# Performance work log

Hardware: AMD Instinct MI355X
Metric: run time of the kernel (lower is better)

## Reference

```python
import math
import jax, jax.numpy as jnp
import numpy as np

N_HEADS = 8
N_POINTS = 4


def bilinear_sample(img, gx, gy):
    """torch F.grid_sample(bilinear, align_corners=True, padding='zeros').
    img: [N,C,H,W]; gx,gy: [N,P] normalized coords (gx -> width axis, gy -> height axis).
    Returns [N,C,P]."""
    N, C, H, W = img.shape
    ix = (gx + 1.0) * 0.5 * (W - 1)
    iy = (gy + 1.0) * 0.5 * (H - 1)
    x0 = jnp.floor(ix); y0 = jnp.floor(iy)
    x1 = x0 + 1.0;      y1 = y0 + 1.0

    def corner(yc, xc, w):
        m = (xc >= 0) & (xc <= W - 1) & (yc >= 0) & (yc <= H - 1)
        xi = jnp.clip(xc, 0, W - 1).astype(jnp.int32)
        yi = jnp.clip(yc, 0, H - 1).astype(jnp.int32)
        v = jax.vmap(lambda im, y, x: im[:, y, x])(img, yi, xi)  # [N,C,P]
        return v * (w * m)[:, None, :]

    return (corner(y0, x0, (x1 - ix) * (y1 - iy))
            + corner(y0, x1, (ix - x0) * (y1 - iy))
            + corner(y1, x0, (x1 - ix) * (iy - y0))
            + corner(y1, x1, (ix - x0) * (iy - y0)))


def forward(query, points, features, cam_M, cam_b, W_off, b_off,
            W_q, b_q, W_k, b_k, W_v, b_v, W_o, b_o):
    B, K, C = query.shape
    ncam = features.shape[0]
    H, W = features.shape[-2:]
    nh, npnt = N_HEADS, N_POINTS
    hd = C // nh
    HW = jnp.asarray([H, W], dtype=query.dtype)

    # camera model: pixel = sigmoid(points @ M^T + b) * [H, W]   -> [ncam,B,K,2]
    px = jax.nn.sigmoid(jnp.einsum('bkj,cij->cbki', points, cam_M)
                        + cam_b[:, None, None, :]) * HW

    # ---- step 1: sample raw features at projected points (per camera) ----
    # original normalizes coord0 by H and coord1 by W (coord0 is grid_sample's x/width axis)
    gx1 = 2.0 * px[..., 0] / H - 1.0          # [ncam,B,K]
    gy1 = 2.0 * px[..., 1] / W - 1.0
    camf = jax.vmap(bilinear_sample)(features, gx1, gy1)   # [ncam,B,C,K]
    camf = jnp.transpose(camf, (1, 3, 0, 2))               # [B,K,ncam,C]

    query_ = query[:, :, None, :] + camf                   # [B,K,ncam,C]
    offsets = (query_ @ W_off.T + b_off).reshape(B, K, ncam, nh, npnt, 2)

    # ---- 1x1 conv key/value projections ----
    kf = (jnp.einsum('cbdhw,ed->cbehw', features, W_k)
          + b_k[None, None, :, None, None]).reshape(ncam, B * nh, hd, H, W)
    vf = (jnp.einsum('cbdhw,ed->cbehw', features, W_v)
          + b_v[None, None, :, None, None]).reshape(ncam, B * nh, hd, H, W)

    # ---- sampling locations with offsets ----
    off = jnp.moveaxis(offsets, 2, 0) / HW                 # [ncam,B,K,nh,np,2]
    pc = px[:, :, :, None, None, :] + off                  # [ncam,B,K,nh,np,2]
    gx = 2.0 * (pc[..., 0] / H) - 1.0
    gy = 2.0 * (pc[..., 1] / W) - 1.0
    # [ncam,B,K,nh,np] -> [ncam, B*nh, K*np]
    gx = jnp.transpose(gx, (0, 1, 3, 2, 4)).reshape(ncam, B * nh, K * npnt)
    gy = jnp.transpose(gy, (0, 1, 3, 2, 4)).reshape(ncam, B * nh, K * npnt)

    keys = jax.vmap(bilinear_sample)(kf, gx, gy)           # [ncam,B*nh,hd,K*np]
    vals = jax.vmap(bilinear_sample)(vf, gx, gy)

    def rearr(t):  # -> [B, nh, K, ncam*np, hd]
        t = t.reshape(ncam, B, nh, hd, K, npnt)
        return jnp.transpose(t, (1, 2, 4, 0, 5, 3)).reshape(B, nh, K, ncam * npnt, hd)

    keys, vals = rearr(keys), rearr(vals)

    q = (query @ W_q.T + b_q).reshape(B, K, nh, hd).transpose(0, 2, 1, 3)  # [B,nh,K,hd]
    logits = jnp.einsum('bhkd,bhkld->bhkl', q, keys) / math.sqrt(hd)
    attn = jax.nn.softmax(logits, axis=-1)
    weighted = jnp.einsum('bhkl,bhkld->bhkd', attn, vals)  # [B,nh,K,hd]
    # faithful to original torch `.view(B, K, embed_dim)` on a [B,nh,K,hd] tensor
    weighted = weighted.reshape(B, K, C)
    return weighted @ W_o.T + b_o


def setup_inputs() -> dict:
    key = jax.random.key(0)
    ks = jax.random.split(key, 16)
    B, K, C = 8, 900, 256
    ncam, H, W = 6, 32, 88
    f = lambda i, shape, s=1.0: jax.random.normal(ks[i], shape, dtype=jnp.float32) * s
    return {
        'query': f(0, (B, K, C)),
        'points': f(1, (B, K, 3)),
        'features': f(2, (ncam, B, C, H, W)),
        'cam_M': f(3, (ncam, 2, 3), 0.5),
        'cam_b': f(4, (ncam, 2), 0.5),
        'W_off': f(5, (2 * N_HEADS * N_POINTS, C), 0.02),
        'b_off': f(6, (2 * N_HEADS * N_POINTS,), 1.0),
        'W_q': f(7, (C, C), 0.02), 'b_q': f(8, (C,), 0.02),
        'W_k': f(9, (C, C), 0.02), 'b_k': f(10, (C,), 0.02),
        'W_v': f(11, (C, C), 0.02), 'b_v': f(12, (C,), 0.02),
        'W_o': f(13, (C, C), 0.02), 'b_o': f(14, (C,), 0.02),
    }


def reference(query, points, features, cam_M, cam_b, W_off, b_off,
              W_q, b_q, W_k, b_k, W_v, b_v, W_o, b_o):
    return forward(query, points, features, cam_M, cam_b, W_off, b_off,
                   W_q, b_q, W_k, b_k, W_v, b_v, W_o, b_o)
```

## Files before the change

### kernel.cpp

```cpp
#include <hip/hip_runtime.h>

typedef __attribute__((ext_vector_type(4))) float f32x4;
typedef __attribute__((ext_vector_type(8))) short bf16x8;
typedef __attribute__((ext_vector_type(4))) unsigned int u32x4;

__device__ __forceinline__ unsigned short f2bf(float f) {
    union { float f; unsigned int u; } x; x.f = f;
    unsigned int u = x.u;
    return (unsigned short)((u + 0x7FFFu + ((u >> 16) & 1u)) >> 16);
}
__device__ __forceinline__ float bf2f(unsigned short b) {
    union { unsigned int u; float f; } x; x.u = ((unsigned int)b) << 16;
    return x.f;
}
__device__ __forceinline__ float u2f(unsigned int u) {
    union { unsigned int u; float f; } x; x.u = u; return x.f;
}


__global__ void prep_all(const float* __restrict__ Wk, const float* __restrict__ bk,
                         const float* __restrict__ Wv, const float* __restrict__ bv,
                         const float* __restrict__ Wq, const float* __restrict__ bq,
                         const float* __restrict__ Woff, const float* __restrict__ boff,
                         unsigned short* __restrict__ Wkv, float* __restrict__ bkv,
                         unsigned short* __restrict__ Woffp,
                         float* __restrict__ Wcat, float* __restrict__ bcat) {
    int i = blockIdx.x * 256 + threadIdx.x;
    if (i < 512 * 256) {
        int n = i >> 8, k = i & 255;
        float v = (n < 256) ? Wk[i] : Wv[i - 65536];
        Wkv[((size_t)(n >> 7) * 8 + (k >> 5)) * 4096 + (n & 127) * 32 + (k & 31)] = f2bf(v);
    }
    if (i < 512) bkv[i] = (i < 256) ? bk[i] : bv[i - 256];
    if (i < 64 * 256) {
        int n = i >> 8, k = i & 255;
        Woffp[(size_t)(k >> 5) * 4096 + n * 32 + (k & 31)] = f2bf(Woff[i]);
    }
    if (i < 320 * 256) Wcat[i] = (i < 65536) ? Wq[i] : Woff[i - 65536];
    if (i < 320) bcat[i] = (i < 256) ? bq[i] : boff[i - 256];
}

__global__ __launch_bounds__(256) void transpose_feat(const float* __restrict__ src,
                                                      unsigned short* __restrict__ dst) {
    __shared__ float tile[32][33];
    int img = blockIdx.z;
    int p0 = blockIdx.x * 32;
    int d0 = blockIdx.y * 32;
    int tx = threadIdx.x & 31, ty = threadIdx.x >> 5;
    const float* s = src + (size_t)img * 256 * 2816;
#pragma unroll
    for (int i = 0; i < 4; i++) tile[ty + 8 * i][tx] = s[(size_t)(d0 + ty + 8 * i) * 2816 + p0 + tx];
    __syncthreads();
    int m = img * 2816 + p0;
    unsigned short* o = dst + ((size_t)(m >> 7) * 8 + (d0 >> 5)) * 4096 + (m & 127) * 32;
#pragma unroll
    for (int i = 0; i < 4; i++) o[(ty + 8 * i) * 32 + tx] = f2bf(tile[tx][ty + 8 * i]);
}

__global__ __launch_bounds__(256) void gemm_kv2(
    const unsigned short* __restrict__ A,
    const unsigned short* __restrict__ Wkv,
    const unsigned short* __restrict__ Woffp,
    const float* __restrict__ bias,
    unsigned short* __restrict__ C,
    float* __restrict__ Foff) {
    __shared__ __align__(16) unsigned short Bl[8192];
    __shared__ __align__(16) unsigned short Ar[3][4096];

    const int tid = threadIdx.x, lane = tid & 63, w = tid >> 6;
    const int lrow = lane & 15, lk = lane >> 4;
    const int lsw = (lane >> 2) * 32 + (((lane & 3) ^ ((lane >> 3) & 3)) * 8);
    const int ckx = ((lrow >> 1) & 3);
    const int bid = blockIdx.x;
    const int wgid = (bid & 7) * 1188 + (bid >> 3);
    const int chunk = wgid / 9, bn = wgid % 9;

    const unsigned short* A0 = A + (size_t)chunk * 32768;
    const unsigned short* Bb = (bn < 8)
        ? Wkv + (size_t)(bn >> 1) * 32768 + (bn & 1) * 2048
        : Woffp;
    const int wof = w * 1024;

#define STAGE_B(HALF)                                                                        \
    {                                                                                        \
        _Pragma("unroll")                                                                    \
        for (int i = 0; i < 4; ++i) {                                                        \
            __builtin_amdgcn_global_load_lds(                                                \
                (const __attribute__((address_space(1))) unsigned int*)(Bb + ((HALF) * 4 + w) * 4096 + i * 512 + lsw), \
                (__attribute__((address_space(3))) unsigned int*)&Bl[w * 2048 + i * 512], 16, 0, 0);                   \
        }                                                                                    \
    }

#define STAGE_STEP(S)                                                                        \
    {                                                                                        \
        __builtin_amdgcn_global_load_lds(                                                    \
            (const __attribute__((address_space(1))) unsigned int*)(A0 + (S) * 4096 + wof + lsw),        \
            (__attribute__((address_space(3))) unsigned int*)&Ar[(S) % 3][wof], 16, 0, 0);   \
        __builtin_amdgcn_global_load_lds(                                                    \
            (const __attribute__((address_space(1))) unsigned int*)(A0 + (S) * 4096 + wof + 512 + lsw),  \
            (__attribute__((address_space(3))) unsigned int*)&Ar[(S) % 3][wof + 512], 16, 0, 0);         \
    }

    STAGE_B(0)
    STAGE_STEP(0) STAGE_STEP(1)
    __syncthreads();

    f32x4 acc[2][4] = {};

#define COMP_STEP(S, NW)                                                                     \
    {                                                                                        \
        asm volatile("s_waitcnt vmcnt(%0)" :: "i"(NW) : "memory");                           \
        bf16x8 bfr[4], af[2];                                                                \
        _Pragma("unroll") for (int j = 0; j < 4; ++j)                                        \
            bfr[j] = *(const bf16x8*)&Bl[((S) & 3) * 2048 + (j * 16 + lrow) * 32 + (lk ^ ckx) * 8]; \
        _Pragma("unroll") for (int i = 0; i < 2; ++i)                                        \
            af[i] = *(const bf16x8*)&Ar[(S) % 3][wof + i * 512 + lrow * 32 + (lk ^ ckx) * 8];\
        if ((S) + 2 < 8) {                                                                   \
            asm volatile("s_waitcnt lgkmcnt(0)" ::: "memory");                               \
            STAGE_STEP((S) + 2)                                                              \
        }                                                                                    \
        _Pragma("unroll") for (int i = 0; i < 2; ++i)                                        \
            _Pragma("unroll") for (int j = 0; j < 4; ++j)                                    \
                acc[i][j] = __builtin_amdgcn_mfma_f32_16x16x32_bf16(af[i], bfr[j], acc[i][j], 0, 0, 0); \
    }

    COMP_STEP(0, 4) COMP_STEP(1, 2) COMP_STEP(2, 2) COMP_STEP(3, 2)
    __syncthreads();
    STAGE_B(1)
    __syncthreads();
    COMP_STEP(4, 4) COMP_STEP(5, 2) COMP_STEP(6, 2) COMP_STEP(7, 0)
#undef COMP_STEP
#undef STAGE_STEP
#undef STAGE_B

    if (bn < 8) {
        unsigned short* Cl = &Ar[0][0];
        __syncthreads();
#pragma unroll
        for (int j = 0; j < 4; ++j) {
            float bs = bias[bn * 64 + j * 16 + lrow];
#pragma unroll
            for (int i = 0; i < 2; ++i)
#pragma unroll
                for (int jj = 0; jj < 4; ++jj)
                    Cl[(w * 32 + i * 16 + lk * 4 + jj) * 64 + j * 16 + lrow] =
                        f2bf(acc[i][j][jj] + bs);
        }
        __syncthreads();
#pragma unroll
        for (int it = 0; it < 4; ++it) {
            int idx = it * 256 + tid;
            int row = idx >> 3, col8 = idx & 7;
            int dstcol = (bn < 4)
                ? (bn * 2 + (col8 >> 2)) * 64 + (col8 & 3) * 8
                : ((bn - 4) * 2 + (col8 >> 2)) * 64 + 32 + (col8 & 3) * 8;
            *(f32x4*)(C + (size_t)(chunk * 128 + row) * 512 + dstcol) =
                *(const f32x4*)&Cl[row * 64 + col8 * 8];
        }
    } else {
#pragma unroll
        for (int i = 0; i < 2; ++i)
#pragma unroll
            for (int j = 0; j < 4; ++j)
#pragma unroll
                for (int jj = 0; jj < 4; ++jj) {
                    int m = chunk * 128 + w * 32 + i * 16 + lk * 4 + jj;
                    Foff[(size_t)m * 64 + j * 16 + lrow] = acc[i][j][jj];
                }
    }
}

template <bool SPLIT, bool C_BF16>
__global__ __launch_bounds__(256) void gemm_bf16(
    const float* __restrict__ A, long long aBatch,
    const float* __restrict__ B, const float* __restrict__ bias,
    void* __restrict__ Cv, long long cBatch,
    int M, int N, int K, int lda) {
    __shared__ __align__(16) unsigned short Ah[64][40];
    __shared__ __align__(16) unsigned short Bh[64][40];
    __shared__ __align__(16) unsigned short Al[(SPLIT ? 64 : 1)][40];
    __shared__ __align__(16) unsigned short Bl[(SPLIT ? 64 : 1)][40];

    const int tid = threadIdx.x;
    const int m0 = blockIdx.x * 64, n0 = blockIdx.y * 64;
    const int batch = blockIdx.z;
    const float* Ab = A + (size_t)batch * aBatch;
    const int lane = tid & 63, wave = tid >> 6;
    const int wr = wave & 1, wc = wave >> 1;
    const int lrow = lane & 15, lk = lane >> 4;

    f32x4 acc[2][2] = {};

    for (int kt = 0; kt < K; kt += 32) {
        if (kt) __syncthreads();
        {
            int c4 = (tid & 7) * 4;
#pragma unroll
            for (int rep = 0; rep < 2; rep++) {
                int r = (tid >> 3) + rep * 32;
                int m = m0 + r; if (m >= M) m = M - 1;
                f32x4 v = *(const f32x4*)(Ab + (size_t)m * lda + kt + c4);
#pragma unroll
                for (int q = 0; q < 4; q++) {
                    unsigned short h = f2bf(v[q]);
                    Ah[r][c4 + q] = h;
                    if (SPLIT) Al[r][c4 + q] = f2bf(v[q] - bf2f(h));
                }
            }
        }
        {
            int c4 = (tid & 7) * 4;
#pragma unroll
            for (int rep = 0; rep < 2; rep++) {
                int r = (tid >> 3) + rep * 32;
                f32x4 v = *(const f32x4*)(B + (size_t)(n0 + r) * K + kt + c4);
#pragma unroll
                for (int q = 0; q < 4; q++) {
                    unsigned short h = f2bf(v[q]);
                    Bh[r][c4 + q] = h;
                    if (SPLIT) Bl[r][c4 + q] = f2bf(v[q] - bf2f(h));
                }
            }
        }
        __syncthreads();

        bf16x8 a_h[2], b_h[2], a_l[2], b_l[2];
#pragma unroll
        for (int i = 0; i < 2; i++) {
            a_h[i] = *(const bf16x8*)&Ah[wr * 32 + i * 16 + lrow][lk * 8];
            b_h[i] = *(const bf16x8*)&Bh[wc * 32 + i * 16 + lrow][lk * 8];
            if (SPLIT) {
                a_l[i] = *(const bf16x8*)&Al[wr * 32 + i * 16 + lrow][lk * 8];
                b_l[i] = *(const bf16x8*)&Bl[wc * 32 + i * 16 + lrow][lk * 8];
            }
        }
#pragma unroll
        for (int i = 0; i < 2; i++)
#pragma unroll
            for (int j = 0; j < 2; j++) {
                acc[i][j] = __builtin_amdgcn_mfma_f32_16x16x32_bf16(a_h[i], b_h[j], acc[i][j], 0, 0, 0);
                if (SPLIT) {
                    acc[i][j] = __builtin_amdgcn_mfma_f32_16x16x32_bf16(a_h[i], b_l[j], acc[i][j], 0, 0, 0);
                    acc[i][j] = __builtin_amdgcn_mfma_f32_16x16x32_bf16(a_l[i], b_h[j], acc[i][j], 0, 0, 0);
                }
            }
    }

#pragma unroll
    for (int i = 0; i < 2; i++)
#pragma unroll
        for (int j = 0; j < 2; j++) {
            int n = n0 + wc * 32 + j * 16 + lrow;
            float bs = bias[n];
#pragma unroll
            for (int jj = 0; jj < 4; jj++) {
                int m = m0 + wr * 32 + i * 16 + lk * 4 + jj;
                if (m < M) {
                    float val = acc[i][j][jj] + bs;
                    if (C_BF16)
                        ((unsigned short*)Cv)[(size_t)batch * cBatch + (size_t)m * N + n] = f2bf(val);
                    else
                        ((float*)Cv)[(size_t)batch * cBatch + (size_t)m * N + n] = val;
                }
            }
        }
}

__global__ __launch_bounds__(512) void attn_kernel(
    const float* __restrict__ qcat, const float* __restrict__ points,
    const float* __restrict__ camM, const float* __restrict__ camb,
    const float* __restrict__ Foff, const unsigned short* __restrict__ kv_t,
    float* __restrict__ S) {
    int bk = blockIdx.x;
    int b = bk / 900, k = bk % 900;
    int h = threadIdx.x >> 6;
    int lane = threadIdx.x & 63;

    __shared__ __align__(16) float        ldsW[8][24][4];
    __shared__ __align__(16) unsigned int ldsI[8][24][4];
    __shared__ float ldsL[8][24];

    if (lane < 24) {
        int cam = lane >> 2, p = lane & 3;
        float pt0 = points[(size_t)bk * 3 + 0];
        float pt1 = points[(size_t)bk * 3 + 1];
        float pt2 = points[(size_t)bk * 3 + 2];
        const float* M = camM + cam * 6;
        float s0 = M[0] * pt0 + M[1] * pt1 + M[2] * pt2 + camb[cam * 2 + 0];
        float s1 = M[3] * pt0 + M[4] * pt1 + M[5] * pt2 + camb[cam * 2 + 1];
        float px0 = (1.f / (1.f + expf(-s0))) * 32.f;
        float px1 = (1.f / (1.f + expf(-s1))) * 88.f;
        {
            float gxb = 2.f * px0 / 32.f - 1.f, gyb = 2.f * px1 / 88.f - 1.f;
            float ixb = (gxb + 1.f) * 0.5f * 87.f;
            float iyb = (gyb + 1.f) * 0.5f * 31.f;
            float xb0 = floorf(ixb), yb0 = floorf(iyb), xb1 = xb0 + 1.f, yb1 = yb0 + 1.f;
            float wxb1 = ixb - xb0, wxb0 = xb1 - ixb, wyb1 = iyb - yb0, wyb0 = yb1 - iyb;
            float mb00 = (xb0 >= 0.f && xb0 <= 87.f && yb0 >= 0.f && yb0 <= 31.f) ? 1.f : 0.f;
            float mb01 = (xb1 >= 0.f && xb1 <= 87.f && yb0 >= 0.f && yb0 <= 31.f) ? 1.f : 0.f;
            float mb10 = (xb0 >= 0.f && xb0 <= 87.f && yb1 >= 0.f && yb1 <= 31.f) ? 1.f : 0.f;
            float mb11 = (xb1 >= 0.f && xb1 <= 87.f && yb1 >= 0.f && yb1 <= 31.f) ? 1.f : 0.f;
            float wb00 = wxb0 * wyb0 * mb00, wb01 = wxb1 * wyb0 * mb01;
            float wb10 = wxb0 * wyb1 * mb10, wb11 = wxb1 * wyb1 * mb11;
            int xib0 = (int)fminf(fmaxf(xb0, 0.f), 87.f);
            int xib1 = (int)fminf(fmaxf(xb1, 0.f), 87.f);
            int yib0 = (int)fminf(fmaxf(yb0, 0.f), 31.f);
            int yib1 = (int)fminf(fmaxf(yb1, 0.f), 31.f);
            size_t base = (size_t)(cam * 8 + b) * 2816;
            const float* f00 = Foff + (base + yib0 * 88 + xib0) * 64;
            const float* f01 = Foff + (base + yib0 * 88 + xib1) * 64;
            const float* f10 = Foff + (base + yib1 * 88 + xib0) * 64;
            const float* f11 = Foff + (base + yib1 * 88 + xib1) * 64;
            int j0 = (h * 4 + p) * 2;
            float o0 = qcat[(size_t)bk * 320 + 256 + j0]
                     + wb00 * f00[j0] + wb01 * f01[j0] + wb10 * f10[j0] + wb11 * f11[j0];
            float o1 = qcat[(size_t)bk * 320 + 256 + j0 + 1]
                     + wb00 * f00[j0 + 1] + wb01 * f01[j0 + 1] + wb10 * f10[j0 + 1] + wb11 * f11[j0 + 1];
            float pc0 = px0 + o0 * (1.f / 32.f);
            float pc1 = px1 + o1 * (1.f / 88.f);
            float gx = 2.f * (pc0 * (1.f / 32.f)) - 1.f;
            float gy = 2.f * (pc1 * (1.f / 88.f)) - 1.f;
            float ix = (gx + 1.f) * 0.5f * 87.f;
            float iy = (gy + 1.f) * 0.5f * 31.f;
            float x0 = floorf(ix), y0 = floorf(iy), x1 = x0 + 1.f, y1 = y0 + 1.f;
            float wx1 = ix - x0, wx0 = x1 - ix, wy1 = iy - y0, wy0 = y1 - iy;
            float m00 = (x0 >= 0.f && x0 <= 87.f && y0 >= 0.f && y0 <= 31.f) ? 1.f : 0.f;
            float m01 = (x1 >= 0.f && x1 <= 87.f && y0 >= 0.f && y0 <= 31.f) ? 1.f : 0.f;
            float m10 = (x0 >= 0.f && x0 <= 87.f && y1 >= 0.f && y1 <= 31.f) ? 1.f : 0.f;
            float m11 = (x1 >= 0.f && x1 <= 87.f && y1 >= 0.f && y1 <= 31.f) ? 1.f : 0.f;
            int xi0 = (int)fminf(fmaxf(x0, 0.f), 87.f);
            int xi1 = (int)fminf(fmaxf(x1, 0.f), 87.f);
            int yi0 = (int)fminf(fmaxf(y0, 0.f), 31.f);
            int yi1 = (int)fminf(fmaxf(y1, 0.f), 31.f);
            unsigned int img = (unsigned int)(cam * 8 + b) * 2816u;
            ldsW[h][lane][0] = wx0 * wy0 * m00;
            ldsW[h][lane][1] = wx1 * wy0 * m01;
            ldsW[h][lane][2] = wx0 * wy1 * m10;
            ldsW[h][lane][3] = wx1 * wy1 * m11;
            ldsI[h][lane][0] = (img + yi0 * 88 + xi0) * 1024u;
            ldsI[h][lane][1] = (img + yi0 * 88 + xi1) * 1024u;
            ldsI[h][lane][2] = (img + yi1 * 88 + xi0) * 1024u;
            ldsI[h][lane][3] = (img + yi1 * 88 + xi1) * 1024u;
        }
    }
    __syncthreads();

    const int p8 = lane >> 3, dlane = lane & 7;
    const int chB = h * 128 + dlane * 16;
    const char* kvb = (const char*)kv_t;

    f32x4 qa = *(const f32x4*)(qcat + (size_t)bk * 320 + h * 32 + (dlane & 3) * 8);
    f32x4 qb = *(const f32x4*)(qcat + (size_t)bk * 320 + h * 32 + (dlane & 3) * 8 + 4);

    float vr[3][8];
    const float inv_sqrt = 0.17677669529663687f;
#pragma unroll
    for (int it = 0; it < 3; ++it) {
        int l = it * 8 + p8;
        f32x4 w = *(const f32x4*)ldsW[h][l];
        unsigned int i0 = ldsI[h][l][0], i1 = ldsI[h][l][1];
        unsigned int i2 = ldsI[h][l][2], i3 = ldsI[h][l][3];
        u32x4 u0 = *(const u32x4*)(kvb + i0 + chB);
        u32x4 u1 = *(const u32x4*)(kvb + i1 + chB);
        u32x4 u2 = *(const u32x4*)(kvb + i2 + chB);
        u32x4 u3 = *(const u32x4*)(kvb + i3 + chB);
#pragma unroll
        for (int q = 0; q < 4; ++q) {
            vr[it][2 * q] = w[0] * u2f(u0[q] << 16) + w[1] * u2f(u1[q] << 16)
                          + w[2] * u2f(u2[q] << 16) + w[3] * u2f(u3[q] << 16);
            vr[it][2 * q + 1] = w[0] * u2f(u0[q] & 0xFFFF0000u) + w[1] * u2f(u1[q] & 0xFFFF0000u)
                              + w[2] * u2f(u2[q] & 0xFFFF0000u) + w[3] * u2f(u3[q] & 0xFFFF0000u);
        }
        float t = qa[0] * vr[it][0] + qa[1] * vr[it][1] + qa[2] * vr[it][2] + qa[3] * vr[it][3]
                + qb[0] * vr[it][4] + qb[1] * vr[it][5] + qb[2] * vr[it][6] + qb[3] * vr[it][7];
        t += __shfl_xor(t, 1);
        t += __shfl_xor(t, 2);
        if (dlane == 0) ldsL[h][l] = t * inv_sqrt;
    }
    __syncthreads();

    float mx = -1e30f;
#pragma unroll
    for (int l = 0; l < 24; l++) mx = fmaxf(mx, ldsL[h][l]);
    float ssum = 0.f;
    float at3[3];
#pragma unroll
    for (int l = 0; l < 24; l++) {
        float e = __expf(ldsL[h][l] - mx);
        ssum += e;
        if ((l & 7) == p8) at3[l >> 3] = e;
    }
    float inv = 1.f / ssum;

    float o[8];
#pragma unroll
    for (int j = 0; j < 8; ++j)
        o[j] = at3[0] * vr[0][j] + at3[1] * vr[1][j] + at3[2] * vr[2][j];
#pragma unroll
    for (int j = 0; j < 8; ++j) {
        o[j] += __shfl_xor(o[j], 8);
        o[j] += __shfl_xor(o[j], 16);
        o[j] += __shfl_xor(o[j], 32);
    }
    if (p8 == 0 && dlane >= 4) {
        int d0 = (dlane - 4) * 8;
        f32x4 v0, v1;
        v0[0] = o[0] * inv; v0[1] = o[1] * inv; v0[2] = o[2] * inv; v0[3] = o[3] * inv;
        v1[0] = o[4] * inv; v1[1] = o[5] * inv; v1[2] = o[6] * inv; v1[3] = o[7] * inv;
        float* dst = &S[(size_t)b * 230400 + (size_t)h * 28800 + k * 32 + d0];
        *(f32x4*)dst = v0;
        *(f32x4*)(dst + 4) = v1;
    }
}

extern "C" void kernel_launch(void* const* d_in, const int* in_sizes, int n_in,
                              void* d_out, int out_size, void* d_ws, size_t ws_size,
                              hipStream_t stream) {
    const float* query    = (const float*)d_in[0];
    const float* points   = (const float*)d_in[1];
    const float* features = (const float*)d_in[2];
    const float* camM     = (const float*)d_in[3];
    const float* camb     = (const float*)d_in[4];
    const float* W_off    = (const float*)d_in[5];
    const float* b_off    = (const float*)d_in[6];
    const float* W_q      = (const float*)d_in[7];
    const float* b_q      = (const float*)d_in[8];
    const float* W_k      = (const float*)d_in[9];
    const float* b_k      = (const float*)d_in[10];
    const float* W_v      = (const float*)d_in[11];
    const float* b_v      = (const float*)d_in[12];
    const float* W_o      = (const float*)d_in[13];
    const float* b_o      = (const float*)d_in[14];

    char* ws = (char*)d_ws;
    unsigned short* feat_t = (unsigned short*)ws; ws += 69206016;
    unsigned short* kv_t   = (unsigned short*)ws; ws += 138412032;
    float* Foff   = (float*)ws; ws += 34603008;
    float* qcat   = (float*)ws; ws += 9216000;
    float* S      = (float*)ws; ws += 7372800;
    unsigned short* Wkv = (unsigned short*)ws; ws += 524288;
    float* bkv    = (float*)ws; ws += 2048;
    unsigned short* Woffp = (unsigned short*)ws; ws += 65536;
    float* Wcat   = (float*)ws; ws += 327680;
    float* bcat   = (float*)ws; ws += 1280;

    prep_all<<<512, 256, 0, stream>>>(W_k, b_k, W_v, b_v, W_q, b_q, W_off, b_off,
                                      Wkv, bkv, Woffp, Wcat, bcat);
    transpose_feat<<<dim3(88, 8, 48), 256, 0, stream>>>(features, feat_t);
    gemm_kv2<<<9504, 256, 0, stream>>>(feat_t, Wkv, Woffp, bkv, kv_t, Foff);
    gemm_bf16<true, false><<<dim3(113, 5, 1), 256, 0, stream>>>(
        query, 0, Wcat, bcat, qcat, 0, 7200, 320, 256, 256);
    attn_kernel<<<7200, 512, 0, stream>>>(qcat, points, camM, camb, Foff, kv_t, S);
    gemm_bf16<true, false><<<dim3(113, 4, 1), 256, 0, stream>>>(
        S, 0, W_o, b_o, d_out, 0, 7200, 256, 256, 256);
}
```

Baseline: 233.0 us.

## Widen KV GEMM tile to compute K and V columns per block

The key/value projection GEMM now computes 128 output columns per workgroup (a K slice and the matching V slice) instead of 64, so each A tile staged in LDS is reused across twice as many MFMAs. The grid shrinks from 9504 to 5280 blocks, and the offset-projection block reuses the same wider path. In exchange, LDS use and accumulator registers double, which may lower occupancy, and the epilogue uses a new column permutation to write interleaved K/V output.

```diff
diff --git a/kernel.cpp b/kernel.cpp
--- a/kernel.cpp
+++ b/kernel.cpp
@@ -64,7 +64,7 @@
     const float* __restrict__ bias,
     unsigned short* __restrict__ C,
     float* __restrict__ Foff) {
-    __shared__ __align__(16) unsigned short Bl[8192];
+    __shared__ __align__(16) unsigned short Bl[16384];
     __shared__ __align__(16) unsigned short Ar[3][4096];
 
     const int tid = threadIdx.x, lane = tid & 63, w = tid >> 6;
@@ -72,12 +72,15 @@
     const int lsw = (lane >> 2) * 32 + (((lane & 3) ^ ((lane >> 3) & 3)) * 8);
     const int ckx = ((lrow >> 1) & 3);
     const int bid = blockIdx.x;
-    const int wgid = (bid & 7) * 1188 + (bid >> 3);
-    const int chunk = wgid / 9, bn = wgid % 9;
+    const int wgid = (bid & 7) * 660 + (bid >> 3);
+    const int chunk = wgid / 5, bn = wgid % 5;
 
     const unsigned short* A0 = A + (size_t)chunk * 32768;
-    const unsigned short* Bb = (bn < 8)
+    const unsigned short* BbK = (bn < 4)
         ? Wkv + (size_t)(bn >> 1) * 32768 + (bn & 1) * 2048
+        : Woffp;
+    const unsigned short* BbV = (bn < 4)
+        ? Wkv + (size_t)((bn + 4) >> 1) * 32768 + ((bn + 4) & 1) * 2048
         : Woffp;
     const int wof = w * 1024;
 
@@ -86,8 +89,14 @@
         _Pragma("unroll")                                                                    \
         for (int i = 0; i < 4; ++i) {                                                        \
             __builtin_amdgcn_global_load_lds(                                                \
-                (const __attribute__((address_space(1))) unsigned int*)(Bb + ((HALF) * 4 + w) * 4096 + i * 512 + lsw), \
-                (__attribute__((address_space(3))) unsigned int*)&Bl[w * 2048 + i * 512], 16, 0, 0);                   \
+                (const __attribute__((address_space(1))) unsigned int*)(BbK + ((HALF) * 4 + w) * 4096 + i * 512 + lsw), \
+                (__attribute__((address_space(3))) unsigned int*)&Bl[w * 4096 + i * 512], 16, 0, 0);                    \
+        }                                                                                    \
+        _Pragma("unroll")                                                                    \
+        for (int i = 0; i < 4; ++i) {                                                        \
+            __builtin_amdgcn_global_load_lds(                                                \
+                (const __attribute__((address_space(1))) unsigned int*)(BbV + ((HALF) * 4 + w) * 4096 + i * 512 + lsw), \
+                (__attribute__((address_space(3))) unsigned int*)&Bl[w * 4096 + 2048 + i * 512], 16, 0, 0);             \
         }                                                                                    \
     }
 
@@ -105,14 +114,16 @@
     STAGE_STEP(0) STAGE_STEP(1)
     __syncthreads();
 
-    f32x4 acc[2][4] = {};
+    f32x4 acc[2][8] = {};
 
 #define COMP_STEP(S, NW)                                                                     \
     {                                                                                        \
         asm volatile("s_waitcnt vmcnt(%0)" :: "i"(NW) : "memory");                           \
-        bf16x8 bfr[4], af[2];                                                                \
+        bf16x8 bfr[8], af[2];                                                                \
         _Pragma("unroll") for (int j = 0; j < 4; ++j)                                        \
-            bfr[j] = *(const bf16x8*)&Bl[((S) & 3) * 2048 + (j * 16 + lrow) * 32 + (lk ^ ckx) * 8]; \
+            bfr[j] = *(const bf16x8*)&Bl[((S) & 3) * 4096 + (j * 16 + lrow) * 32 + (lk ^ ckx) * 8];          \
+        _Pragma("unroll") for (int j = 0; j < 4; ++j)                                        \
+            bfr[4 + j] = *(const bf16x8*)&Bl[((S) & 3) * 4096 + 2048 + (j * 16 + lrow) * 32 + (lk ^ ckx) * 8]; \
         _Pragma("unroll") for (int i = 0; i < 2; ++i)                                        \
             af[i] = *(const bf16x8*)&Ar[(S) % 3][wof + i * 512 + lrow * 32 + (lk ^ ckx) * 8];\
         if ((S) + 2 < 8) {                                                                   \
@@ -120,7 +131,7 @@
             STAGE_STEP((S) + 2)                                                              \
         }                                                                                    \
         _Pragma("unroll") for (int i = 0; i < 2; ++i)                                        \
-            _Pragma("unroll") for (int j = 0; j < 4; ++j)                                    \
+            _Pragma("unroll") for (int j = 0; j < 8; ++j)                                    \
                 acc[i][j] = __builtin_amdgcn_mfma_f32_16x16x32_bf16(af[i], bfr[j], acc[i][j], 0, 0, 0); \
     }
 
@@ -133,29 +144,28 @@
 #undef STAGE_STEP
 #undef STAGE_B
 
-    if (bn < 8) {
-        unsigned short* Cl = &Ar[0][0];
+    if (bn < 4) {
+        unsigned short* Cl = &Bl[0];
         __syncthreads();
 #pragma unroll
-        for (int j = 0; j < 4; ++j) {
-            float bs = bias[bn * 64 + j * 16 + lrow];
+        for (int j = 0; j < 8; ++j) {
+            float bs = (j < 4) ? bias[bn * 64 + j * 16 + lrow]
+                               : bias[(bn + 4) * 64 + (j - 4) * 16 + lrow];
 #pragma unroll
             for (int i = 0; i < 2; ++i)
 #pragma unroll
                 for (int jj = 0; jj < 4; ++jj)
-                    Cl[(w * 32 + i * 16 + lk * 4 + jj) * 64 + j * 16 + lrow] =
+                    Cl[(w * 32 + i * 16 + lk * 4 + jj) * 128 + j * 16 + lrow] =
                         f2bf(acc[i][j][jj] + bs);
         }
         __syncthreads();
 #pragma unroll
-        for (int it = 0; it < 4; ++it) {
+        for (int it = 0; it < 8; ++it) {
             int idx = it * 256 + tid;
-            int row = idx >> 3, col8 = idx & 7;
-            int dstcol = (bn < 4)
-                ? (bn * 2 + (col8 >> 2)) * 64 + (col8 & 3) * 8
-                : ((bn - 4) * 2 + (col8 >> 2)) * 64 + 32 + (col8 & 3) * 8;
-            *(f32x4*)(C + (size_t)(chunk * 128 + row) * 512 + dstcol) =
-                *(const f32x4*)&Cl[row * 64 + col8 * 8];
+            int px = idx >> 4, d = idx & 15;
+            int s = (d < 4) ? d : (d < 8) ? d + 4 : (d < 12) ? d - 4 : d;
+            *(f32x4*)(C + (size_t)(chunk * 128 + px) * 512 + bn * 128 + d * 8) =
+                *(const f32x4*)&Cl[px * 128 + s * 8];
         }
     } else {
 #pragma unroll
@@ -447,7 +457,7 @@
     prep_all<<<512, 256, 0, stream>>>(W_k, b_k, W_v, b_v, W_q, b_q, W_off, b_off,
                                       Wkv, bkv, Woffp, Wcat, bcat);
     transpose_feat<<<dim3(88, 8, 48), 256, 0, stream>>>(features, feat_t);
-    gemm_kv2<<<9504, 256, 0, stream>>>(feat_t, Wkv, Woffp, bkv, kv_t, Foff);
+    gemm_kv2<<<5280, 256, 0, stream>>>(feat_t, Wkv, Woffp, bkv, kv_t, Foff);
     gemm_bf16<true, false><<<dim3(113, 5, 1), 256, 0, stream>>>(
         query, 0, Wcat, bcat, qcat, 0, 7200, 320, 256, 256);
     attn_kernel<<<7200, 512, 0, stream>>>(qcat, points, camM, camb, Foff, kv_t, S);
```

Measured after the change: 231.2 us (median of 2 runs). Within noise of the previous version (-0.8%).

## Restructure KV/offset GEMM to keep A tile resident and stream all weights

Applied to the files above, without the earlier changes.

Replaces the 9504-block KV/offset projection GEMM, where each block computed a 128x64 output tile, with 2112 blocks. Each block loads a 64-row slab of features (full K=256) into LDS once and streams all 576 output columns of repacked weights through a 4-slot ring buffer. A K/V column group's bias-added bf16 results are written directly after each 64-column unit, and the offset columns come last in fp32. This removes the redundant reloads of the A tile across the nine column blocks, at the cost of more sequential work per block, uncoalesced direct stores without LDS staging, and fewer blocks in flight.

```diff
diff --git a/kernel.cpp b/kernel.cpp
--- a/kernel.cpp
+++ b/kernel.cpp
@@ -22,19 +22,21 @@
                          const float* __restrict__ Wv, const float* __restrict__ bv,
                          const float* __restrict__ Wq, const float* __restrict__ bq,
                          const float* __restrict__ Woff, const float* __restrict__ boff,
-                         unsigned short* __restrict__ Wkv, float* __restrict__ bkv,
-                         unsigned short* __restrict__ Woffp,
+                         unsigned short* __restrict__ Wall, float* __restrict__ ball,
                          float* __restrict__ Wcat, float* __restrict__ bcat) {
     int i = blockIdx.x * 256 + threadIdx.x;
-    if (i < 512 * 256) {
-        int n = i >> 8, k = i & 255;
-        float v = (n < 256) ? Wk[i] : Wv[i - 65536];
-        Wkv[((size_t)(n >> 7) * 8 + (k >> 5)) * 4096 + (n & 127) * 32 + (k & 31)] = f2bf(v);
-    }
-    if (i < 512) bkv[i] = (i < 256) ? bk[i] : bv[i - 256];
-    if (i < 64 * 256) {
-        int n = i >> 8, k = i & 255;
-        Woffp[(size_t)(k >> 5) * 4096 + n * 32 + (k & 31)] = f2bf(Woff[i]);
+    {
+        int slab = i >> 11, r = (i >> 5) & 63, c = i & 31;
+        int u = slab >> 3, kt = slab & 7;
+        float v;
+        if (u < 8) v = (r < 32) ? Wk[(u * 32 + r) * 256 + kt * 32 + c]
+                                : Wv[(u * 32 + r - 32) * 256 + kt * 32 + c];
+        else       v = Woff[r * 256 + kt * 32 + c];
+        Wall[i] = f2bf(v);
+    }
+    if (i < 576) {
+        int u = i >> 6, r = i & 63;
+        ball[i] = (u < 8) ? ((r < 32) ? bk[u * 32 + r] : bv[u * 32 + r - 32]) : 0.f;
     }
     if (i < 320 * 256) Wcat[i] = (i < 65536) ? Wq[i] : Woff[i - 65536];
     if (i < 320) bcat[i] = (i < 256) ? bq[i] : boff[i - 256];
@@ -57,117 +59,90 @@
     for (int i = 0; i < 4; i++) o[(ty + 8 * i) * 32 + tx] = f2bf(tile[tx][ty + 8 * i]);
 }
 
-__global__ __launch_bounds__(256) void gemm_kv2(
+__global__ __launch_bounds__(256) void gemm_fused(
     const unsigned short* __restrict__ A,
-    const unsigned short* __restrict__ Wkv,
-    const unsigned short* __restrict__ Woffp,
-    const float* __restrict__ bias,
+    const unsigned short* __restrict__ Wall,
+    const float* __restrict__ ball,
     unsigned short* __restrict__ C,
     float* __restrict__ Foff) {
-    __shared__ __align__(16) unsigned short Bl[8192];
-    __shared__ __align__(16) unsigned short Ar[3][4096];
+    __shared__ __align__(16) unsigned short Alds[16384];
+    __shared__ __align__(16) unsigned short Bring[8192];
 
     const int tid = threadIdx.x, lane = tid & 63, w = tid >> 6;
     const int lrow = lane & 15, lk = lane >> 4;
     const int lsw = (lane >> 2) * 32 + (((lane & 3) ^ ((lane >> 3) & 3)) * 8);
     const int ckx = ((lrow >> 1) & 3);
     const int bid = blockIdx.x;
-    const int wgid = (bid & 7) * 1188 + (bid >> 3);
-    const int chunk = wgid / 9, bn = wgid % 9;
-
-    const unsigned short* A0 = A + (size_t)chunk * 32768;
-    const unsigned short* Bb = (bn < 8)
-        ? Wkv + (size_t)(bn >> 1) * 32768 + (bn & 1) * 2048
-        : Woffp;
-    const int wof = w * 1024;
-
-#define STAGE_B(HALF)                                                                        \
-    {                                                                                        \
-        _Pragma("unroll")                                                                    \
-        for (int i = 0; i < 4; ++i) {                                                        \
-            __builtin_amdgcn_global_load_lds(                                                \
-                (const __attribute__((address_space(1))) unsigned int*)(Bb + ((HALF) * 4 + w) * 4096 + i * 512 + lsw), \
-                (__attribute__((address_space(3))) unsigned int*)&Bl[w * 2048 + i * 512], 16, 0, 0);                   \
-        }                                                                                    \
-    }
-
-#define STAGE_STEP(S)                                                                        \
-    {                                                                                        \
-        __builtin_amdgcn_global_load_lds(                                                    \
-            (const __attribute__((address_space(1))) unsigned int*)(A0 + (S) * 4096 + wof + lsw),        \
-            (__attribute__((address_space(3))) unsigned int*)&Ar[(S) % 3][wof], 16, 0, 0);   \
-        __builtin_amdgcn_global_load_lds(                                                    \
-            (const __attribute__((address_space(1))) unsigned int*)(A0 + (S) * 4096 + wof + 512 + lsw),  \
-            (__attribute__((address_space(3))) unsigned int*)&Ar[(S) % 3][wof + 512], 16, 0, 0);         \
-    }
-
-    STAGE_B(0)
-    STAGE_STEP(0) STAGE_STEP(1)
+    const int wgid = (bid & 7) * 264 + (bid >> 3);
+    const unsigned short* A0 = A + (size_t)(wgid >> 1) * 32768 + (wgid & 1) * 2048;
+
+#pragma unroll
+    for (int kk = 0; kk < 2; ++kk) {
+        int kt = w * 2 + kk;
+#pragma unroll
+        for (int i = 0; i < 4; ++i) {
+            __builtin_amdgcn_global_load_lds(
+                (const __attribute__((address_space(1))) unsigned int*)(A0 + kt * 4096 + i * 512 + lsw),
+                (__attribute__((address_space(3))) unsigned int*)&Alds[kt * 2048 + i * 512], 16, 0, 0);
+        }
+    }
+
+#define STAGE_B(S3)                                                                          \
+    __builtin_amdgcn_global_load_lds(                                                        \
+        (const __attribute__((address_space(1))) unsigned int*)(Wall + (S3) * 2048 + w * 512 + lsw), \
+        (__attribute__((address_space(3))) unsigned int*)&Bring[((S3) & 3) * 2048 + w * 512], 16, 0, 0);
+
+    STAGE_B(0) STAGE_B(1) STAGE_B(2)
     __syncthreads();
 
-    f32x4 acc[2][4] = {};
+    f32x4 acc[4] = {};
 
 #define COMP_STEP(S, NW)                                                                     \
     {                                                                                        \
         asm volatile("s_waitcnt vmcnt(%0)" :: "i"(NW) : "memory");                           \
-        bf16x8 bfr[4], af[2];                                                                \
-        _Pragma("unroll") for (int j = 0; j < 4; ++j)                                        \
-            bfr[j] = *(const bf16x8*)&Bl[((S) & 3) * 2048 + (j * 16 + lrow) * 32 + (lk ^ ckx) * 8]; \
-        _Pragma("unroll") for (int i = 0; i < 2; ++i)                                        \
-            af[i] = *(const bf16x8*)&Ar[(S) % 3][wof + i * 512 + lrow * 32 + (lk ^ ckx) * 8];\
-        if ((S) + 2 < 8) {                                                                   \
+        bf16x8 bfr, af[4];                                                                   \
+        bfr = *(const bf16x8*)&Bring[((S) & 3) * 2048 + w * 512 + lrow * 32 + (lk ^ ckx) * 8]; \
+        _Pragma("unroll") for (int i = 0; i < 4; ++i)                                        \
+            af[i] = *(const bf16x8*)&Alds[((S) & 7) * 2048 + (i * 16 + lrow) * 32 + (lk ^ ckx) * 8]; \
+        if ((S) + 3 < 72) {                                                                  \
             asm volatile("s_waitcnt lgkmcnt(0)" ::: "memory");                               \
-            STAGE_STEP((S) + 2)                                                              \
+            STAGE_B((S) + 3)                                                                 \
         }                                                                                    \
-        _Pragma("unroll") for (int i = 0; i < 2; ++i)                                        \
-            _Pragma("unroll") for (int j = 0; j < 4; ++j)                                    \
-                acc[i][j] = __builtin_amdgcn_mfma_f32_16x16x32_bf16(af[i], bfr[j], acc[i][j], 0, 0, 0); \
-    }
-
-    COMP_STEP(0, 4) COMP_STEP(1, 2) COMP_STEP(2, 2) COMP_STEP(3, 2)
-    __syncthreads();
-    STAGE_B(1)
-    __syncthreads();
-    COMP_STEP(4, 4) COMP_STEP(5, 2) COMP_STEP(6, 2) COMP_STEP(7, 0)
+        _Pragma("unroll") for (int i = 0; i < 4; ++i)                                        \
+            acc[i] = __builtin_amdgcn_mfma_f32_16x16x32_bf16(af[i], bfr, acc[i], 0, 0, 0);   \
+    }
+
+#define EPI_KV(U)                                                                            \
+    {                                                                                        \
+        float bs = ball[(U) * 64 + w * 16 + lrow];                                           \
+        _Pragma("unroll") for (int i = 0; i < 4; ++i) {                                      \
+            _Pragma("unroll") for (int jj = 0; jj < 4; ++jj)                                 \
+                C[(size_t)(wgid * 64 + i * 16 + lk * 4 + jj) * 512 + (U) * 64 + w * 16 + lrow] = \
+                    f2bf(acc[i][jj] + bs);                                                   \
+            acc[i] = (f32x4){0.f, 0.f, 0.f, 0.f};                                            \
+        }                                                                                    \
+    }
+
+#define UNIT(U)                                                                              \
+    COMP_STEP((U) * 8 + 0, 2) COMP_STEP((U) * 8 + 1, 2) COMP_STEP((U) * 8 + 2, 2)            \
+    COMP_STEP((U) * 8 + 3, 2) COMP_STEP((U) * 8 + 4, 2) COMP_STEP((U) * 8 + 5, 2)            \
+    COMP_STEP((U) * 8 + 6, 2) COMP_STEP((U) * 8 + 7, 2) EPI_KV(U)
+
+    UNIT(0) UNIT(1) UNIT(2) UNIT(3) UNIT(4) UNIT(5) UNIT(6) UNIT(7)
+
+    COMP_STEP(64, 2) COMP_STEP(65, 2) COMP_STEP(66, 2) COMP_STEP(67, 2)
+    COMP_STEP(68, 2) COMP_STEP(69, 2) COMP_STEP(70, 1) COMP_STEP(71, 0)
+    {
+#pragma unroll
+        for (int i = 0; i < 4; ++i)
+#pragma unroll
+            for (int jj = 0; jj < 4; ++jj)
+                Foff[(size_t)(wgid * 64 + i * 16 + lk * 4 + jj) * 64 + w * 16 + lrow] = acc[i][jj];
+    }
+#undef UNIT
+#undef EPI_KV
 #undef COMP_STEP
-#undef STAGE_STEP
 #undef STAGE_B
-
-    if (bn < 8) {
-        unsigned short* Cl = &Ar[0][0];
-        __syncthreads();
-#pragma unroll
-        for (int j = 0; j < 4; ++j) {
-            float bs = bias[bn * 64 + j * 16 + lrow];
-#pragma unroll
-            for (int i = 0; i < 2; ++i)
-#pragma unroll
-                for (int jj = 0; jj < 4; ++jj)
-                    Cl[(w * 32 + i * 16 + lk * 4 + jj) * 64 + j * 16 + lrow] =
-                        f2bf(acc[i][j][jj] + bs);
-        }
-        __syncthreads();
-#pragma unroll
-        for (int it = 0; it < 4; ++it) {
-            int idx = it * 256 + tid;
-            int row = idx >> 3, col8 = idx & 7;
-            int dstcol = (bn < 4)
-                ? (bn * 2 + (col8 >> 2)) * 64 + (col8 & 3) * 8
-                : ((bn - 4) * 2 + (col8 >> 2)) * 64 + 32 + (col8 & 3) * 8;
-            *(f32x4*)(C + (size_t)(chunk * 128 + row) * 512 + dstcol) =
-                *(const f32x4*)&Cl[row * 64 + col8 * 8];
-        }
-    } else {
-#pragma unroll
-        for (int i = 0; i < 2; ++i)
-#pragma unroll
-            for (int j = 0; j < 4; ++j)
-#pragma unroll
-                for (int jj = 0; jj < 4; ++jj) {
-                    int m = chunk * 128 + w * 32 + i * 16 + lk * 4 + jj;
-                    Foff[(size_t)m * 64 + j * 16 + lrow] = acc[i][j][jj];
-                }
-    }
 }
 
 template <bool SPLIT, bool C_BF16>
@@ -438,16 +413,15 @@
     float* Foff   = (float*)ws; ws += 34603008;
     float* qcat   = (float*)ws; ws += 9216000;
     float* S      = (float*)ws; ws += 7372800;
-    unsigned short* Wkv = (unsigned short*)ws; ws += 524288;
-    float* bkv    = (float*)ws; ws += 2048;
-    unsigned short* Woffp = (unsigned short*)ws; ws += 65536;
+    unsigned short* Wall = (unsigned short*)ws; ws += 294912;
+    float* ball   = (float*)ws; ws += 4096;
     float* Wcat   = (float*)ws; ws += 327680;
     float* bcat   = (float*)ws; ws += 1280;
 
-    prep_all<<<512, 256, 0, stream>>>(W_k, b_k, W_v, b_v, W_q, b_q, W_off, b_off,
-                                      Wkv, bkv, Woffp, Wcat, bcat);
+    prep_all<<<576, 256, 0, stream>>>(W_k, b_k, W_v, b_v, W_q, b_q, W_off, b_off,
+                                      Wall, ball, Wcat, bcat);
     transpose_feat<<<dim3(88, 8, 48), 256, 0, stream>>>(features, feat_t);
-    gemm_kv2<<<9504, 256, 0, stream>>>(feat_t, Wkv, Woffp, bkv, kv_t, Foff);
+    gemm_fused<<<2112, 256, 0, stream>>>(feat_t, Wall, ball, kv_t, Foff);
     gemm_bf16<true, false><<<dim3(113, 5, 1), 256, 0, stream>>>(
         query, 0, Wcat, bcat, qcat, 0, 7200, 320, 256, 256);
     attn_kernel<<<7200, 512, 0, stream>>>(qcat, points, camM, camb, Foff, kv_t, S);
```

After: 220.2 us, median of 2. 5.5% less time.
